# Kernel tuning notes

Measured on AMD Instinct MI355X. Metric: run time of the kernel, lower is better.

The kernel has to match this reference:

```python
import jax, jax.numpy as jnp
import numpy as np

B, T, H, N_HEADS, HEAD_D = 16, 512, 1024, 16, 64
N_SKILLS, N_ITEMS = 50, 1000
VOCAB = 4 + 2 * N_ITEMS  # 2004
LN_EPS = 1e-3            # keras LayerNormalization default
PAD_NEG = -float(2 ** 32)


def position_encoding(length, hidden):
    # official transformer get_position_encoding: [sin | cos], then interleaved
    half = hidden // 2
    pos = jnp.arange(length, dtype=jnp.float32)[:, None]
    log_inc = np.log(1e4) / (half - 1)
    inv_ts = jnp.exp(jnp.arange(half, dtype=jnp.float32) * -log_inc)
    ang = pos * inv_ts[None, :]  # [T, H/2]
    pe = jnp.zeros((length, hidden), dtype=jnp.float32)
    pe = pe.at[:, 0::2].set(jnp.sin(ang))
    pe = pe.at[:, 1::2].set(jnp.cos(ang))
    return pe


def setup_inputs() -> dict:
    key = jax.random.key(0)
    ks = jax.random.split(key, 12)
    rng = np.random.default_rng(0)
    # binary Q-matrix [skills, items]; ensure every item has >=1 skill
    Qb = (rng.random((N_SKILLS, N_ITEMS)) < 0.1).astype(np.float32)
    Qb[rng.integers(0, N_SKILLS, size=N_ITEMS), np.arange(N_ITEMS)] = 1.0
    s = 0.02
    return {
        'prob_x': jax.random.randint(ks[0], (B, T), 4, VOCAB, dtype=jnp.int32),
        'prob_y2': jax.random.randint(ks[1], (B, T), 4, VOCAB, dtype=jnp.int32),
        'emb': jax.random.normal(ks[2], (VOCAB, H), jnp.float32) * s,
        'wq': jax.random.normal(ks[3], (H, N_HEADS, HEAD_D), jnp.float32) * s,
        'wk': jax.random.normal(ks[4], (H, N_HEADS, HEAD_D), jnp.float32) * s,
        'wv': jax.random.normal(ks[5], (H, N_HEADS, HEAD_D), jnp.float32) * s,
        'wo': jax.random.normal(ks[6], (N_HEADS, HEAD_D, H), jnp.float32) * s,
        'ln_gamma': jnp.ones((H,), jnp.float32),
        'ln_beta': jnp.zeros((H,), jnp.float32),
        'w_hid': jax.random.normal(ks[7], (H, 2 * N_SKILLS), jnp.float32) * s,
        'b_hid': jnp.zeros((2 * N_SKILLS,), jnp.float32),
        'w_skill': jax.random.normal(ks[8], (2 * N_SKILLS, N_SKILLS), jnp.float32) * s,
        'b_skill': jnp.zeros((N_SKILLS,), jnp.float32),
        'w_prob': jax.random.normal(ks[9], (N_SKILLS, N_ITEMS), jnp.float32) * s,
        'b_prob': jnp.zeros((N_ITEMS,), jnp.float32),
        'q_matrix': jnp.asarray(Qb),
    }


def reference(prob_x, prob_y2, emb, wq, wk, wv, wo, ln_gamma, ln_beta,
              w_hid, b_hid, w_skill, b_skill, w_prob, b_prob, q_matrix):
    Bq, Tq = prob_x.shape
    pid = (prob_x - 4) // 2        # item ids [B,T]
    next_pid = (prob_y2 - 4) // 2  # [B,T]

    x = emb[prob_x] + position_encoding(Tq, emb.shape[1])  # [B,T,H]

    # QKV projections (DenseEinsum, no bias)
    q = jnp.einsum('bth,hnd->btnd', x, wq) * (HEAD_D ** -0.5)
    k = jnp.einsum('bth,hnd->btnd', x, wk)
    v = jnp.einsum('bth,hnd->btnd', x, wv)

    logits = jnp.einsum('btnd,bfnd->bnft', k, q)  # [B,N,F,T]

    # causal future mask: 0 on/below diag, -inf above (1 - exp(1/tri - 1))
    causal = jnp.where(jnp.tril(jnp.ones((Tq, Tq), bool)), 0.0, -jnp.inf)
    logits = logits + causal[None, None]

    # item-item common-skill mask: -inf where items share no skill, 0 otherwise
    qtq = q_matrix.T @ q_matrix  # [I,I]
    items_items = jnp.where(qtq > 0, 0.0, -jnp.inf)
    sub = items_items[pid[:, 1:, None], pid[:, None, 1:]]  # [B,T-1,T-1]
    csm = jnp.pad(sub, ((0, 0), (1, 0), (1, 0)), constant_values=PAD_NEG)
    logits = logits + csm[:, None]  # broadcast over heads

    weights = jax.nn.softmax(logits, axis=-1)  # [B,N,F,T]
    attn = jnp.einsum('bnft,btnd->bfnd', weights, v)
    attn = jnp.einsum('bfnd,ndh->bfh', attn, wo)

    # add & layer-norm (keras default eps=1e-3)
    y = x + attn
    mu = jnp.mean(y, axis=-1, keepdims=True)
    var = jnp.var(y, axis=-1, keepdims=True)
    y = (y - mu) * jax.lax.rsqrt(var + LN_EPS) * ln_gamma + ln_beta

    h = jax.nn.relu(y @ w_hid + b_hid)
    skills = h @ w_skill + b_skill
    problems = jax.nn.sigmoid(skills @ w_prob + b_prob)  # [B,T,I]
    # einsum('abi,abi->ab', problems, one_hot(next_pid)) == gather
    out = jnp.take_along_axis(problems, next_pid[..., None], axis=-1)[..., 0]
    return out
```

## Files before the change

kernel.cpp:

```cpp
#include <hip/hip_runtime.h>
#include <hip/hip_bf16.h>

#define Bb 16
#define Tt 512
#define Hh 1024
#define NHd 16
#define HD 64
#define BT (Bb*Tt)
#define NSK 50
#define NIT 1000

typedef __attribute__((ext_vector_type(8))) short bf16x8;
typedef __attribute__((ext_vector_type(4))) float f32x4;
typedef unsigned short u16;
typedef unsigned int u32;
typedef unsigned long long u64;

__device__ inline u16 f2bf(float x){
  union { float f; u32 u; } v; v.f = x;
  u32 r = v.u + 0x7fffu + ((v.u >> 16) & 1u);
  return (u16)(r >> 16);
}
__device__ inline float bf2f(u32 u){
  union { u32 uu; float f; } v; v.uu = u << 16; return v.f;
}
__device__ inline u32 pack2bf(float lo, float hi){
  return (u32)f2bf(lo) | ((u32)f2bf(hi) << 16);
}
__device__ inline void gload_lds16(const void* g, void* l){
  __builtin_amdgcn_global_load_lds(
    (const __attribute__((address_space(1))) u32*)g,
    (__attribute__((address_space(3))) u32*)l, 16, 0, 0);
}

__global__ __launch_bounds__(256) void k_wT_all(
    const float* __restrict__ wq, const float* __restrict__ wk,
    const float* __restrict__ wv, const float* __restrict__ wo,
    const float* __restrict__ wh, const float* __restrict__ gamma,
    const float* __restrict__ beta,
    const int* __restrict__ prob_x, const float* __restrict__ qm,
    const float* __restrict__ wp,
    u16* __restrict__ wqkvT, u16* __restrict__ woT, u16* __restrict__ whT,
    float2* __restrict__ uvp, u64* __restrict__ pmask, float* __restrict__ wpt){
  int z = blockIdx.z;
  int tid = threadIdx.x;
  if (z == 5){
    if (blockIdx.y) return;
    int i = blockIdx.x*256 + tid;
    int pid = (prob_x[i] - 4) >> 1;
    u64 m = 0ull;
    #pragma unroll
    for (int s = 0; s < NSK; s++)
      if (qm[s*NIT + pid] != 0.f) m |= (1ull << s);
    pmask[i] = m;
    return;
  }
  if (z == 6){
    int blk = blockIdx.y*32 + blockIdx.x;
    if (blk >= 250) return;
    int p = blk*4 + (tid >> 6), lane = tid & 63;
    if (lane < NSK) wpt[(size_t)p*64 + lane] = wp[(size_t)lane*NIT + p];
    return;
  }
  const float* src; u16* dst; int C = 1024; float scale = 1.f; bool useg = false;
  if      (z == 0){ src = wq; dst = wqkvT;                       scale = 0.125f; }
  else if (z == 1){ src = wk; dst = wqkvT + (size_t)1024*1024; }
  else if (z == 2){ src = wv; dst = wqkvT + (size_t)2*1024*1024; }
  else if (z == 3){ src = wo; dst = woT; }
  else            { src = wh; dst = whT; C = 100; useg = true; if (blockIdx.x >= 4) return; }

  __shared__ float tile[32][33];
  int tx = tid & 31, ty = tid >> 5;
  int c0 = blockIdx.x*32, r0 = blockIdx.y*32;
  #pragma unroll
  for (int i = 0; i < 32; i += 8){
    int r = r0 + ty + i, cc = c0 + tx;
    tile[ty+i][tx] = (cc < C) ? src[(size_t)r*C + cc] : 0.f;
  }
  __syncthreads();
  float gmul = useg ? gamma[r0 + tx] : scale;
  #pragma unroll
  for (int i = 0; i < 32; i += 8){
    int cc = c0 + ty + i, rr = r0 + tx;
    dst[(size_t)cc*1024 + rr] = f2bf(tile[tx][ty+i] * gmul);
  }
  if (useg && tid < 32){
    int j = tid;
    float us = 0.f, vs = 0.f;
    #pragma unroll
    for (int k = 0; k < 32; k++){
      float wv2 = tile[k][j];
      us += gamma[r0 + k] * wv2;
      vs += beta[r0 + k] * wv2;
    }
    uvp[(size_t)blockIdx.y*128 + c0 + j] = make_float2(us, vs);
  }
}

__global__ __launch_bounds__(256) void k_build_x2(
    const int* __restrict__ prob_x, const float* __restrict__ emb,
    u16* __restrict__ xb){
  int bt = blockIdx.x, tid = threadIdx.x;
  int t = bt & (Tt-1);
  int ix = prob_x[bt];
  int h = tid*4;
  float4 e = *(const float4*)(emb + (size_t)ix*Hh + h);
  const float LOG_INC = 0.0180241495f;
  int j0 = h >> 1;
  float a0 = (float)t * __expf(-(float)j0 * LOG_INC);
  float a1 = (float)t * __expf(-(float)(j0+1) * LOG_INC);
  alignas(8) u16 tmp[4] = { f2bf(e.x + __sinf(a0)), f2bf(e.y + __cosf(a0)),
                            f2bf(e.z + __sinf(a1)), f2bf(e.w + __cosf(a1)) };
  *(uint2*)(xb + (size_t)bt*Hh + h) = *(const uint2*)tmp;
}

__global__ __launch_bounds__(256) void k_gemm_qkv(
    const u16* __restrict__ A, const u16* __restrict__ Bt,
    u16* __restrict__ qb, u16* __restrict__ kb, u16* __restrict__ vtb)
{
  __shared__ u16 sA[128*64];
  __shared__ u16 sB[128*64];
  const int tid = threadIdx.x, w = tid >> 6, lane = tid & 63;
  const int c = lane & 15, g = lane >> 4;
  int lin = blockIdx.y*24 + blockIdx.x;
  int id2 = (lin & 7)*192 + (lin >> 3);
  int bx = id2 % 24, by = id2 / 24;
  const int row0 = by*128, col0 = bx*128;
  const int wr = w >> 1, wc = w & 1;
  const int srl = lane >> 3, scb = lane & 7;

  f32x4 acc[4][4];
  #pragma unroll
  for (int mi = 0; mi < 4; mi++)
    #pragma unroll
    for (int ni = 0; ni < 4; ni++) acc[mi][ni] = (f32x4){0.f,0.f,0.f,0.f};

  for (int k0 = 0; k0 < 1024; k0 += 64){
    __syncthreads();
    #pragma unroll
    for (int i = 0; i < 4; i++){
      int arow = 32*w + 8*i + srl;
      int kblk = scb ^ (arow & 7);
      gload_lds16(A  + (size_t)(row0 + arow)*1024 + k0 + kblk*8,
                  (char*)sA + w*4096 + i*1024);
      gload_lds16(Bt + (size_t)(col0 + arow)*1024 + k0 + kblk*8,
                  (char*)sB + w*4096 + i*1024);
    }
    __syncthreads();

    #pragma unroll
    for (int kh = 0; kh < 2; kh++){
      bf16x8 af[4], bf[4];
      #pragma unroll
      for (int mi = 0; mi < 4; mi++){
        int r = 64*wr + 16*mi + c;
        af[mi] = *(const bf16x8*)((char*)sA + r*128 + (((4*kh + g) ^ (r & 7))*16));
      }
      #pragma unroll
      for (int ni = 0; ni < 4; ni++){
        int r = 64*wc + 16*ni + c;
        bf[ni] = *(const bf16x8*)((char*)sB + r*128 + (((4*kh + g) ^ (r & 7))*16));
      }
      #pragma unroll
      for (int mi = 0; mi < 4; mi++)
        #pragma unroll
        for (int ni = 0; ni < 4; ni++)
          acc[mi][ni] = __builtin_amdgcn_mfma_f32_16x16x32_bf16(af[mi], bf[ni], acc[mi][ni], 0, 0, 0);
    }
  }

  int seg = col0 >> 10;
  int colL0 = col0 & 1023;
  if (seg < 2){
    u16* C = seg ? kb : qb;
    #pragma unroll
    for (int mi = 0; mi < 4; mi++){
      int m0 = row0 + 64*wr + 16*mi + 4*g;
      int bb = m0 >> 9, t0 = m0 & (Tt-1);
      #pragma unroll
      for (int ni = 0; ni < 4; ni++){
        int col = colL0 + 64*wc + 16*ni + c;
        int hd_ = col >> 6, d_ = col & 63;
        u16* base = C + (((size_t)bb*NHd + hd_)*Tt + t0)*HD + d_;
        #pragma unroll
        for (int r = 0; r < 4; r++) base[(size_t)r*HD] = f2bf(acc[mi][ni][r]);
      }
    }
  } else {
    #pragma unroll
    for (int mi = 0; mi < 4; mi++){
      int m0 = row0 + 64*wr + 16*mi + 4*g;
      int bb = m0 >> 9, t0 = m0 & (Tt-1);
      #pragma unroll
      for (int ni = 0; ni < 4; ni++){
        int col = colL0 + 64*wc + 16*ni + c;
        int hd_ = col >> 6, d_ = col & 63;
        alignas(8) u16 tmp[4];
        #pragma unroll
        for (int r = 0; r < 4; r++) tmp[r] = f2bf(acc[mi][ni][r]);
        *(uint2*)(vtb + (((size_t)bb*NHd + hd_)*HD + d_)*Tt + t0) = *(const uint2*)tmp;
      }
    }
  }
}

__global__ __launch_bounds__(256) void k_gemm_wo(
    const u16* __restrict__ A, const u16* __restrict__ Bt,
    u16* __restrict__ C, const u16* __restrict__ res, float2* __restrict__ stats)
{
  __shared__ u16 sA[128*64];
  __shared__ u16 sB[128*64];
  const int tid = threadIdx.x, w = tid >> 6, lane = tid & 63;
  const int c = lane & 15, g = lane >> 4;
  int lin = blockIdx.y*8 + blockIdx.x;
  int id2 = (lin & 7)*64 + (lin >> 3);
  int bx = id2 & 7, by = id2 >> 3;
  const int row0 = by*128, col0 = bx*128;
  const int wr = w >> 1, wc = w & 1;
  const int srl = lane >> 3, scb = lane & 7;

  f32x4 acc[4][4];
  #pragma unroll
  for (int mi = 0; mi < 4; mi++)
    #pragma unroll
    for (int ni = 0; ni < 4; ni++) acc[mi][ni] = (f32x4){0.f,0.f,0.f,0.f};

  for (int k0 = 0; k0 < 1024; k0 += 64){
    __syncthreads();
    #pragma unroll
    for (int i = 0; i < 4; i++){
      int arow = 32*w + 8*i + srl;
      int kblk = scb ^ (arow & 7);
      gload_lds16(A  + (size_t)(row0 + arow)*1024 + k0 + kblk*8,
                  (char*)sA + w*4096 + i*1024);
      gload_lds16(Bt + (size_t)(col0 + arow)*1024 + k0 + kblk*8,
                  (char*)sB + w*4096 + i*1024);
    }
    __syncthreads();

    #pragma unroll
    for (int kh = 0; kh < 2; kh++){
      bf16x8 af[4], bf[4];
      #pragma unroll
      for (int mi = 0; mi < 4; mi++){
        int r = 64*wr + 16*mi + c;
        af[mi] = *(const bf16x8*)((char*)sA + r*128 + (((4*kh + g) ^ (r & 7))*16));
      }
      #pragma unroll
      for (int ni = 0; ni < 4; ni++){
        int r = 64*wc + 16*ni + c;
        bf[ni] = *(const bf16x8*)((char*)sB + r*128 + (((4*kh + g) ^ (r & 7))*16));
      }
      #pragma unroll
      for (int mi = 0; mi < 4; mi++)
        #pragma unroll
        for (int ni = 0; ni < 4; ni++)
          acc[mi][ni] = __builtin_amdgcn_mfma_f32_16x16x32_bf16(af[mi], bf[ni], acc[mi][ni], 0, 0, 0);
    }
  }

  __syncthreads();
  float s1[4][4], s2[4][4];
  #pragma unroll
  for (int mi = 0; mi < 4; mi++)
    #pragma unroll
    for (int r = 0; r < 4; r++){ s1[mi][r] = 0.f; s2[mi][r] = 0.f; }

  #pragma unroll
  for (int mi = 0; mi < 4; mi++){
    int m0 = row0 + 64*wr + 16*mi + 4*g;
    #pragma unroll
    for (int ni = 0; ni < 4; ni++){
      int col = col0 + 64*wc + 16*ni + c;
      #pragma unroll
      for (int r = 0; r < 4; r++){
        size_t idx = (size_t)(m0 + r)*Hh + col;
        float yv = acc[mi][ni][r] + bf2f((u32)res[idx]);
        C[idx] = f2bf(yv);
        s1[mi][r] += yv; s2[mi][r] += yv*yv;
      }
    }
  }
  #pragma unroll
  for (int mi = 0; mi < 4; mi++)
    #pragma unroll
    for (int r = 0; r < 4; r++){
      #pragma unroll
      for (int off = 1; off < 16; off <<= 1){
        s1[mi][r] += __shfl_xor(s1[mi][r], off);
        s2[mi][r] += __shfl_xor(s2[mi][r], off);
      }
    }
  float (*sStat)[2][2] = (float(*)[2][2])sA;
  if (c == 0){
    #pragma unroll
    for (int mi = 0; mi < 4; mi++)
      #pragma unroll
      for (int r = 0; r < 4; r++){
        int ml = 64*wr + 16*mi + 4*g + r;
        sStat[ml][wc][0] = s1[mi][r];
        sStat[ml][wc][1] = s2[mi][r];
      }
  }
  __syncthreads();
  if (tid < 128){
    float a = sStat[tid][0][0] + sStat[tid][1][0];
    float b = sStat[tid][0][1] + sStat[tid][1][1];
    stats[(size_t)(row0 + tid)*8 + bx] = make_float2(a, b);
  }
}

__global__ __launch_bounds__(256) void k_gemm_hidden(
    const u16* __restrict__ A, const u16* __restrict__ Bt,
    const float2* __restrict__ stats, const float2* __restrict__ uvp,
    const float* __restrict__ b_hid, u16* __restrict__ C)
{
  __shared__ u16 sA[32*64];
  __shared__ u16 sB[128*64];
  __shared__ float sMu[32][2];
  __shared__ float2 sUV[128];
  const int tid = threadIdx.x, w = tid >> 6, lane = tid & 63;
  const int c = lane & 15, g = lane >> 4;
  const int row0 = blockIdx.x*32;
  const int srl = lane >> 3, scb = lane & 7;

  if (tid < 32){
    float m = 0.f, q = 0.f;
    #pragma unroll
    for (int cb = 0; cb < 8; cb++){
      float2 s = stats[(size_t)(row0 + tid)*8 + cb];
      m += s.x; q += s.y;
    }
    float mu = m * (1.f/Hh);
    float var = q * (1.f/Hh) - mu*mu;
    sMu[tid][0] = mu;
    sMu[tid][1] = rsqrtf(var + 1e-3f);
  }
  if (tid < 128){
    float us = 0.f, vs = 0.f;
    #pragma unroll 8
    for (int cb = 0; cb < 32; cb++){
      float2 p = uvp[(size_t)cb*128 + tid];
      us += p.x; vs += p.y;
    }
    float2 r = make_float2(0.f, 0.f);
    if (tid < 100){ r.x = us; r.y = vs + b_hid[tid]; }
    sUV[tid] = r;
  }

  f32x4 acc[2][2];
  #pragma unroll
  for (int mi = 0; mi < 2; mi++)
    #pragma unroll
    for (int ni = 0; ni < 2; ni++) acc[mi][ni] = (f32x4){0.f,0.f,0.f,0.f};

  for (int k0 = 0; k0 < 1024; k0 += 64){
    __syncthreads();
    {
      int arow = 8*w + srl;
      int kblk = scb ^ (arow & 7);
      gload_lds16(A + (size_t)(row0 + arow)*1024 + k0 + kblk*8,
                  (char*)sA + w*1024);
      #pragma unroll
      for (int i = 0; i < 4; i++){
        int brow = 32*w + 8*i + srl;
        int kb2 = scb ^ (brow & 7);
        gload_lds16(Bt + (size_t)brow*1024 + k0 + kb2*8,
                    (char*)sB + w*4096 + i*1024);
      }
    }
    __syncthreads();

    #pragma unroll
    for (int kh = 0; kh < 2; kh++){
      bf16x8 af[2], bf[2];
      #pragma unroll
      for (int mi = 0; mi < 2; mi++){
        int r = 16*mi + c;
        af[mi] = *(const bf16x8*)((char*)sA + r*128 + (((4*kh + g) ^ (r & 7))*16));
      }
      #pragma unroll
      for (int ni = 0; ni < 2; ni++){
        int r = 32*w + 16*ni + c;
        bf[ni] = *(const bf16x8*)((char*)sB + r*128 + (((4*kh + g) ^ (r & 7))*16));
      }
      #pragma unroll
      for (int mi = 0; mi < 2; mi++)
        #pragma unroll
        for (int ni = 0; ni < 2; ni++)
          acc[mi][ni] = __builtin_amdgcn_mfma_f32_16x16x32_bf16(af[mi], bf[ni], acc[mi][ni], 0, 0, 0);
    }
  }

  #pragma unroll
  for (int mi = 0; mi < 2; mi++){
    #pragma unroll
    for (int ni = 0; ni < 2; ni++){
      int col = 32*w + 16*ni + c;
      float2 uvv = sUV[col];
      #pragma unroll
      for (int r = 0; r < 4; r++){
        int ml = 16*mi + 4*g + r;
        float mu = sMu[ml][0], inv = sMu[ml][1];
        float h = fmaxf(inv*(acc[mi][ni][r] - mu*uvv.x) + uvv.y, 0.f);
        C[(size_t)(row0 + ml)*128 + col] = f2bf(h);
      }
    }
  }
}

__global__ __launch_bounds__(256, 3) void k_flash(
    const u16* __restrict__ qb, const u16* __restrict__ kb,
    const u16* __restrict__ vtb, const u64* __restrict__ pmask,
    u16* __restrict__ o)
{
  __shared__ u16 sK[2][64*64];
  __shared__ u16 sV[2][64*64];
  __shared__ u16 sP[4][32*64];

  const int tid = threadIdx.x;
  const int w = tid >> 6, lane = tid & 63;
  const int c = lane & 15, g = lane >> 4;
  const int bn = blockIdx.x;
  const int Fblk = 3 - blockIdx.y;
  const int b = bn >> 4, n = bn & 15;
  const int f0w = Fblk*128 + w*32;

  bf16x8 qf[2][2];
  #pragma unroll
  for (int fb = 0; fb < 2; fb++){
    const u16* qrow = qb + ((size_t)bn*Tt + f0w + 16*fb + c)*HD + 8*g;
    qf[fb][0] = *(const bf16x8*)(qrow);
    qf[fb][1] = *(const bf16x8*)(qrow + 32);
  }

  const u64* pmb = pmask + b*Tt;
  int frow[2]; u64 mf[2];
  #pragma unroll
  for (int fb = 0; fb < 2; fb++){ frow[fb] = f0w + 16*fb + c; mf[fb] = pmb[frow[fb]]; }

  f32x4 O[2][4];
  #pragma unroll
  for (int fb = 0; fb < 2; fb++)
    #pragma unroll
    for (int dt = 0; dt < 4; dt++) O[fb][dt] = (f32x4){0.f,0.f,0.f,0.f};
  float m_run[2] = {-1e30f, -1e30f};
  float l_run[2] = {0.f, 0.f};

  const char* kbase = (const char*)(kb + (size_t)bn*Tt*HD);
  const char* vbase = (const char*)(vtb + (size_t)bn*HD*Tt);
  char* sPw = (char*)(sP[w]);

  const int srow0 = 16*w + (lane >> 3);
  const int scb = lane & 7;

  #define STAGE(buf, T0)                                                          \
    {                                                                             \
      _Pragma("unroll")                                                           \
      for (int i = 0; i < 2; i++){                                                \
        int row = srow0 + 8*i;                                                    \
        int cb = scb ^ (row & 7);                                                 \
        gload_lds16(kbase + (size_t)((T0) + row)*128 + cb*16,                     \
                    (char*)sK[buf] + w*2048 + i*1024);                            \
        gload_lds16(vbase + (size_t)row*1024 + (T0)*2 + cb*16,                    \
                    (char*)sV[buf] + w*2048 + i*1024);                            \
      }                                                                           \
    }

  const int nT = 2*Fblk + 2;
  STAGE(0, 0)
  __syncthreads();
  int cur = 0;

  for (int it = 0; it < nT; ++it){
    const int t0 = it * 64;
    if (it + 1 < nT) STAGE(cur^1, (it+1)*64)

    if (t0 <= f0w + 31){
      const char* sKc = (const char*)sK[cur];
      const char* sVc = (const char*)sV[cur];

      f32x4 S[2][4];
      __builtin_amdgcn_s_setprio(1);
      #pragma unroll
      for (int ts = 0; ts < 4; ts++){
        int tl = ts*16 + c;
        const char* kr = sKc + tl*128;
        int sw = (tl & 7) << 4;
        bf16x8 kf0 = *(const bf16x8*)(kr + ((g*16) ^ sw));
        bf16x8 kf1 = *(const bf16x8*)(kr + ((64 + g*16) ^ sw));
        #pragma unroll
        for (int fb = 0; fb < 2; fb++){
          f32x4 a = (f32x4){0.f,0.f,0.f,0.f};
          a = __builtin_amdgcn_mfma_f32_16x16x32_bf16(kf0, qf[fb][0], a, 0, 0, 0);
          a = __builtin_amdgcn_mfma_f32_16x16x32_bf16(kf1, qf[fb][1], a, 0, 0, 0);
          S[fb][ts] = a;
        }
      }
      __builtin_amdgcn_s_setprio(0);

      u64 pmt[4][4];
      #pragma unroll
      for (int ts = 0; ts < 4; ts++){
        const u64* pp = pmb + t0 + 16*ts + 4*g;
        pmt[ts][0] = pp[0]; pmt[ts][1] = pp[1];
        pmt[ts][2] = pp[2]; pmt[ts][3] = pp[3];
      }

      #pragma unroll
      for (int fb = 0; fb < 2; fb++){
        int f = frow[fb];
        u64 mfr = mf[fb];
        #pragma unroll
        for (int ts = 0; ts < 4; ts++){
          #pragma unroll
          for (int r = 0; r < 4; r++){
            int t = t0 + 16*ts + 4*g + r;
            bool ok = (f == 0) ? (t == 0)
                     : (t > 0 && t <= f && ((pmt[ts][r] & mfr) != 0ull));
            if (!ok) S[fb][ts][r] = -1e30f;
          }
        }
        float mx = -1e30f;
        #pragma unroll
        for (int ts = 0; ts < 4; ts++)
          #pragma unroll
          for (int r = 0; r < 4; r++) mx = fmaxf(mx, S[fb][ts][r]);
        mx = fmaxf(mx, __shfl_xor(mx, 16));
        mx = fmaxf(mx, __shfl_xor(mx, 32));
        float mnew = fmaxf(m_run[fb], mx);
        float al = __expf(m_run[fb] - mnew);
        m_run[fb] = mnew;
        l_run[fb] *= al;
        #pragma unroll
        for (int dt = 0; dt < 4; dt++) O[fb][dt] *= al;

        int prow = 16*fb + c;
        int swz = (prow & 7) << 4;
        float lsum = 0.f;
        #pragma unroll
        for (int ts = 0; ts < 4; ts++){
          float p0 = __expf(S[fb][ts][0] - mnew);
          float p1 = __expf(S[fb][ts][1] - mnew);
          float p2 = __expf(S[fb][ts][2] - mnew);
          float p3 = __expf(S[fb][ts][3] - mnew);
          lsum += (p0 + p1) + (p2 + p3);
          uint2 dw = { pack2bf(p0, p1), pack2bf(p2, p3) };
          *(uint2*)(sPw + prow*128 + ((32*ts + 8*g) ^ swz)) = dw;
        }
        l_run[fb] += lsum;
      }

      bf16x8 pa[2][2];
      #pragma unroll
      for (int fb = 0; fb < 2; fb++){
        int prow = 16*fb + c;
        int swz = (prow & 7) << 4;
        const char* pr = sPw + prow*128;
        pa[fb][0] = *(const bf16x8*)(pr + ((16*g) ^ swz));
        pa[fb][1] = *(const bf16x8*)(pr + ((64 + 16*g) ^ swz));
      }
      __builtin_amdgcn_s_setprio(1);
      #pragma unroll
      for (int dt = 0; dt < 4; dt++){
        int vl = dt*16 + c;
        const char* vr = sVc + vl*128;
        int swv = (vl & 7) << 4;
        bf16x8 vf0 = *(const bf16x8*)(vr + ((g*16) ^ swv));
        bf16x8 vf1 = *(const bf16x8*)(vr + ((64 + g*16) ^ swv));
        #pragma unroll
        for (int fb = 0; fb < 2; fb++){
          O[fb][dt] = __builtin_amdgcn_mfma_f32_16x16x32_bf16(vf0, pa[fb][0], O[fb][dt], 0, 0, 0);
          O[fb][dt] = __builtin_amdgcn_mfma_f32_16x16x32_bf16(vf1, pa[fb][1], O[fb][dt], 0, 0, 0);
        }
      }
      __builtin_amdgcn_s_setprio(0);
    }

    __syncthreads();
    cur ^= 1;
  }
  #undef STAGE

  #pragma unroll
  for (int fb = 0; fb < 2; fb++){
    float l = l_run[fb];
    l += __shfl_xor(l, 16);
    l += __shfl_xor(l, 32);
    float inv = 1.f / l;
    u16* ob = o + ((size_t)(b*Tt + frow[fb]))*Hh + n*HD;
    #pragma unroll
    for (int dt = 0; dt < 4; dt++){
      alignas(8) u16 tmp[4];
      #pragma unroll
      for (int r = 0; r < 4; r++) tmp[r] = f2bf(O[fb][dt][r] * inv);
      *(uint2*)(ob + dt*16 + 4*g) = *(const uint2*)tmp;
    }
  }
}

__global__ __launch_bounds__(256) void k_tail(
    const u16* __restrict__ hidden, const int* __restrict__ prob_y2,
    const float* __restrict__ w_skill, const float* __restrict__ b_skill,
    const float* __restrict__ wpt, const float* __restrict__ b_prob,
    float* __restrict__ out)
{
  __shared__ float shid[4][104];
  int w = threadIdx.x >> 6, lane = threadIdx.x & 63;
  int row = blockIdx.x*4 + w;
  if (lane < 50){
    u32 hp = *(const u32*)(hidden + (size_t)row*128 + 2*lane);
    shid[w][2*lane]   = bf2f(hp & 0xffffu);
    shid[w][2*lane+1] = bf2f(hp >> 16);
  }
  __syncthreads();
  float s = 0.f;
  if (lane < 50){
    s = b_skill[lane];
    #pragma unroll 4
    for (int i = 0; i < 100; i++) s += shid[w][i] * w_skill[i*NSK + lane];
  }
  int np = (prob_y2[row] - 4) >> 1;
  float z = (lane < 50) ? s * wpt[(size_t)np*64 + lane] : 0.f;
  #pragma unroll
  for (int off = 1; off < 64; off <<= 1) z += __shfl_xor(z, off);
  if (lane == 0) out[row] = 1.f/(1.f + expf(-(z + b_prob[np])));
}

extern "C" void kernel_launch(void* const* d_in, const int* in_sizes, int n_in,
                              void* d_out, int out_size, void* d_ws, size_t ws_size,
                              hipStream_t stream)
{
  const int*   prob_x   = (const int*)d_in[0];
  const int*   prob_y2  = (const int*)d_in[1];
  const float* emb      = (const float*)d_in[2];
  const float* wq       = (const float*)d_in[3];
  const float* wk       = (const float*)d_in[4];
  const float* wv       = (const float*)d_in[5];
  const float* wo       = (const float*)d_in[6];
  const float* ln_g     = (const float*)d_in[7];
  const float* ln_b     = (const float*)d_in[8];
  const float* w_hid    = (const float*)d_in[9];
  const float* b_hid    = (const float*)d_in[10];
  const float* w_skill  = (const float*)d_in[11];
  const float* b_skill  = (const float*)d_in[12];
  const float* w_prob   = (const float*)d_in[13];
  const float* b_prob   = (const float*)d_in[14];
  const float* q_matrix = (const float*)d_in[15];
  float* out = (float*)d_out;

  char* ws = (char*)d_ws;
  const size_t M16 = (size_t)BT*Hh*2;
  u16*   xb     = (u16*)(ws);
  u16*   qb     = (u16*)(ws + M16);
  u16*   kb     = (u16*)(ws + 2*M16);
  u16*   vtb    = (u16*)(ws + 3*M16);
  u16*   att    = (u16*)(ws + 4*M16);
  u16*   y      = qb;
  u16*   hidden = kb;
  char*  aux    = ws + 5*M16;
  u16*   wqkvT  = (u16*)(aux);
  u16*   woT    = wqkvT + (size_t)3*1024*1024;
  u16*   whT    = woT + (size_t)1024*1024;
  float* wpt    = (float*)(whT + (size_t)128*1024);
  u64*   pmask  = (u64*)(wpt + (size_t)NIT*64);
  float2* stats = (float2*)((char*)pmask + (size_t)BT*8);
  float2* uvp   = (float2*)((char*)stats + (size_t)BT*8*sizeof(float2));

  k_wT_all<<<dim3(32,32,7), 256, 0, stream>>>(wq, wk, wv, wo, w_hid, ln_g, ln_b,
                                              prob_x, q_matrix, w_prob,
                                              wqkvT, woT, whT, uvp, pmask, wpt);
  k_build_x2<<<BT, 256, 0, stream>>>(prob_x, emb, xb);

  k_gemm_qkv<<<dim3(24,64), 256, 0, stream>>>(xb, wqkvT, qb, kb, vtb);

  k_flash<<<dim3(Bb*NHd, 4), 256, 0, stream>>>(qb, kb, vtb, pmask, att);

  k_gemm_wo<<<dim3(8,64), 256, 0, stream>>>(att, woT, y, xb, stats);

  k_gemm_hidden<<<256, 256, 0, stream>>>(y, whT, stats, uvp, b_hid, hidden);

  k_tail<<<BT/4, 256, 0, stream>>>(hidden, prob_y2, w_skill, b_skill, wpt, b_prob, out);
}
```

Baseline: 180.7 us.

## Rewrite QKV GEMM with 256x256 tiles, 8 waves, double-buffered LDS pipeline

```diff
diff --git a/kernel.cpp b/kernel.cpp
--- a/kernel.cpp
+++ b/kernel.cpp
@@ -114,72 +114,139 @@
   *(uint2*)(xb + (size_t)bt*Hh + h) = *(const uint2*)tmp;
 }
 
-__global__ __launch_bounds__(256) void k_gemm_qkv(
+#define MFMA_(d, va, vb) d = __builtin_amdgcn_mfma_f32_16x16x32_bf16(va, vb, d, 0, 0, 0)
+
+__global__ __launch_bounds__(512, 2) void k_gemm_qkv8(
     const u16* __restrict__ A, const u16* __restrict__ Bt,
     u16* __restrict__ qb, u16* __restrict__ kb, u16* __restrict__ vtb)
 {
-  __shared__ u16 sA[128*64];
-  __shared__ u16 sB[128*64];
+  extern __shared__ char lds[];
   const int tid = threadIdx.x, w = tid >> 6, lane = tid & 63;
   const int c = lane & 15, g = lane >> 4;
-  int lin = blockIdx.y*24 + blockIdx.x;
-  int id2 = (lin & 7)*192 + (lin >> 3);
-  int bx = id2 % 24, by = id2 / 24;
-  const int row0 = by*128, col0 = bx*128;
-  const int wr = w >> 1, wc = w & 1;
+  const int wm = w >> 2, wn = w & 3;
   const int srl = lane >> 3, scb = lane & 7;
 
-  f32x4 acc[4][4];
-  #pragma unroll
-  for (int mi = 0; mi < 4; mi++)
+  int lin = blockIdx.x;
+  int swz = (lin & 7)*48 + (lin >> 3);
+  int bx = swz % 12, by = swz / 12;
+  const int row0 = by*256, col0 = bx*256;
+
+  f32x4 acc[8][4];
+  #pragma unroll
+  for (int mi = 0; mi < 8; mi++)
     #pragma unroll
     for (int ni = 0; ni < 4; ni++) acc[mi][ni] = (f32x4){0.f,0.f,0.f,0.f};
 
-  for (int k0 = 0; k0 < 1024; k0 += 64){
-    __syncthreads();
-    #pragma unroll
-    for (int i = 0; i < 4; i++){
-      int arow = 32*w + 8*i + srl;
-      int kblk = scb ^ (arow & 7);
-      gload_lds16(A  + (size_t)(row0 + arow)*1024 + k0 + kblk*8,
-                  (char*)sA + w*4096 + i*1024);
-      gload_lds16(Bt + (size_t)(col0 + arow)*1024 + k0 + kblk*8,
-                  (char*)sB + w*4096 + i*1024);
-    }
-    __syncthreads();
-
-    #pragma unroll
-    for (int kh = 0; kh < 2; kh++){
-      bf16x8 af[4], bf[4];
-      #pragma unroll
-      for (int mi = 0; mi < 4; mi++){
-        int r = 64*wr + 16*mi + c;
-        af[mi] = *(const bf16x8*)((char*)sA + r*128 + (((4*kh + g) ^ (r & 7))*16));
-      }
-      #pragma unroll
-      for (int ni = 0; ni < 4; ni++){
-        int r = 64*wc + 16*ni + c;
-        bf[ni] = *(const bf16x8*)((char*)sB + r*128 + (((4*kh + g) ^ (r & 7))*16));
-      }
-      #pragma unroll
-      for (int mi = 0; mi < 4; mi++)
-        #pragma unroll
-        for (int ni = 0; ni < 4; ni++)
-          acc[mi][ni] = __builtin_amdgcn_mfma_f32_16x16x32_bf16(af[mi], bf[ni], acc[mi][ni], 0, 0, 0);
-    }
-  }
+  #define STAGEH(buf, mat, h, k0)                                               \
+    do {                                                                        \
+      const u16* _s = (mat) ? Bt : A;                                           \
+      int _b0 = (mat) ? col0 : row0;                                            \
+      char* _d = lds + (buf)*65536 + (mat)*32768 + (h)*16384 + w*2048;          \
+      int _kb = scb ^ srl;                                                      \
+      gload_lds16(_s + (size_t)(_b0 + (h)*128 + w*16 + srl)*1024 + (k0) + _kb*8,\
+                  _d);                                                          \
+      gload_lds16(_s + (size_t)(_b0 + (h)*128 + w*16 + 8 + srl)*1024 + (k0) + _kb*8,\
+                  _d + 1024);                                                   \
+    } while (0)
+
+  #define AFRAG(buf, mi, kh)                                                    \
+    (*(const bf16x8*)(lds + (buf)*65536 + (128*wm + 16*(mi) + c)*128 +          \
+                      ((((kh)*4 + g) ^ (c & 7))*16)))
+  #define BFRAG(buf, ni, kh)                                                    \
+    (*(const bf16x8*)(lds + (buf)*65536 + 32768 + (64*wn + 16*(ni) + c)*128 +   \
+                      ((((kh)*4 + g) ^ (c & 7))*16)))
+
+  STAGEH(0, 0, 0, 0); STAGEH(0, 0, 1, 0);
+  STAGEH(0, 1, 0, 0); STAGEH(0, 1, 1, 0);
+
+  bf16x8 af[4], bfr[4];
+
+  for (int kt = 0; kt < 16; ++kt){
+    const int buf = kt & 1, nbuf = buf ^ 1;
+    const int k0n = (kt + 1)*64;
+    const bool pf = (kt < 15);
+
+    if (pf){
+      STAGEH(nbuf, 0, 0, k0n);
+      asm volatile("s_waitcnt vmcnt(2)" ::: "memory");
+    } else {
+      asm volatile("s_waitcnt vmcnt(0)" ::: "memory");
+    }
+    __builtin_amdgcn_sched_barrier(0);
+    __builtin_amdgcn_s_barrier();
+    #pragma unroll
+    for (int mi = 0; mi < 4; mi++) af[mi] = AFRAG(buf, mi, 0);
+    #pragma unroll
+    for (int ni = 0; ni < 4; ni++) bfr[ni] = BFRAG(buf, ni, 0);
+    asm volatile("s_waitcnt lgkmcnt(0)" ::: "memory");
+    __builtin_amdgcn_sched_barrier(0);
+    __builtin_amdgcn_s_setprio(1);
+    #pragma unroll
+    for (int mi = 0; mi < 4; mi++)
+      #pragma unroll
+      for (int ni = 0; ni < 4; ni++) MFMA_(acc[mi][ni], af[mi], bfr[ni]);
+    __builtin_amdgcn_s_setprio(0);
+    __builtin_amdgcn_s_barrier();
+
+    #pragma unroll
+    for (int mi = 0; mi < 4; mi++) af[mi] = AFRAG(buf, 4 + mi, 0);
+    if (pf) STAGEH(nbuf, 0, 1, k0n);
+    __builtin_amdgcn_s_barrier();
+    asm volatile("s_waitcnt lgkmcnt(0)" ::: "memory");
+    __builtin_amdgcn_sched_barrier(0);
+    __builtin_amdgcn_s_setprio(1);
+    #pragma unroll
+    for (int mi = 0; mi < 4; mi++)
+      #pragma unroll
+      for (int ni = 0; ni < 4; ni++) MFMA_(acc[4 + mi][ni], af[mi], bfr[ni]);
+    __builtin_amdgcn_s_setprio(0);
+    __builtin_amdgcn_s_barrier();
+
+    #pragma unroll
+    for (int mi = 0; mi < 4; mi++) af[mi] = AFRAG(buf, mi, 1);
+    #pragma unroll
+    for (int ni = 0; ni < 4; ni++) bfr[ni] = BFRAG(buf, ni, 1);
+    if (pf) STAGEH(nbuf, 1, 0, k0n);
+    __builtin_amdgcn_s_barrier();
+    asm volatile("s_waitcnt lgkmcnt(0)" ::: "memory");
+    __builtin_amdgcn_sched_barrier(0);
+    __builtin_amdgcn_s_setprio(1);
+    #pragma unroll
+    for (int mi = 0; mi < 4; mi++)
+      #pragma unroll
+      for (int ni = 0; ni < 4; ni++) MFMA_(acc[mi][ni], af[mi], bfr[ni]);
+    __builtin_amdgcn_s_setprio(0);
+    __builtin_amdgcn_s_barrier();
+
+    #pragma unroll
+    for (int mi = 0; mi < 4; mi++) af[mi] = AFRAG(buf, 4 + mi, 1);
+    if (pf) STAGEH(nbuf, 1, 1, k0n);
+    __builtin_amdgcn_s_barrier();
+    asm volatile("s_waitcnt lgkmcnt(0)" ::: "memory");
+    __builtin_amdgcn_sched_barrier(0);
+    __builtin_amdgcn_s_setprio(1);
+    #pragma unroll
+    for (int mi = 0; mi < 4; mi++)
+      #pragma unroll
+      for (int ni = 0; ni < 4; ni++) MFMA_(acc[4 + mi][ni], af[mi], bfr[ni]);
+    __builtin_amdgcn_s_setprio(0);
+    __builtin_amdgcn_s_barrier();
+  }
+  #undef STAGEH
+  #undef AFRAG
+  #undef BFRAG
 
   int seg = col0 >> 10;
   int colL0 = col0 & 1023;
   if (seg < 2){
     u16* C = seg ? kb : qb;
     #pragma unroll
-    for (int mi = 0; mi < 4; mi++){
-      int m0 = row0 + 64*wr + 16*mi + 4*g;
+    for (int mi = 0; mi < 8; mi++){
+      int m0 = row0 + 128*wm + 16*mi + 4*g;
       int bb = m0 >> 9, t0 = m0 & (Tt-1);
       #pragma unroll
       for (int ni = 0; ni < 4; ni++){
-        int col = colL0 + 64*wc + 16*ni + c;
+        int col = colL0 + 64*wn + 16*ni + c;
         int hd_ = col >> 6, d_ = col & 63;
         u16* base = C + (((size_t)bb*NHd + hd_)*Tt + t0)*HD + d_;
         #pragma unroll
@@ -188,12 +255,12 @@
     }
   } else {
     #pragma unroll
-    for (int mi = 0; mi < 4; mi++){
-      int m0 = row0 + 64*wr + 16*mi + 4*g;
+    for (int mi = 0; mi < 8; mi++){
+      int m0 = row0 + 128*wm + 16*mi + 4*g;
       int bb = m0 >> 9, t0 = m0 & (Tt-1);
       #pragma unroll
       for (int ni = 0; ni < 4; ni++){
-        int col = colL0 + 64*wc + 16*ni + c;
+        int col = colL0 + 64*wn + 16*ni + c;
         int hd_ = col >> 6, d_ = col & 63;
         alignas(8) u16 tmp[4];
         #pragma unroll
@@ -672,7 +739,7 @@
                                               wqkvT, woT, whT, uvp, pmask, wpt);
   k_build_x2<<<BT, 256, 0, stream>>>(prob_x, emb, xb);
 
-  k_gemm_qkv<<<dim3(24,64), 256, 0, stream>>>(xb, wqkvT, qb, kb, vtb);
+  k_gemm_qkv8<<<384, 512, 131072, stream>>>(xb, wqkvT, qb, kb, vtb);
 
   k_flash<<<dim3(Bb*NHd, 4), 256, 0, stream>>>(qb, kb, vtb, pmask, att);
 
```

After: 175.5 us. 1.03x faster.

## Use triple-buffered 128x256 GEMM core with 512 threads for QKV and Wo

Applied to the files above, without the earlier changes.

```diff
diff --git a/kernel.cpp b/kernel.cpp
--- a/kernel.cpp
+++ b/kernel.cpp
@@ -114,72 +114,108 @@
   *(uint2*)(xb + (size_t)bt*Hh + h) = *(const uint2*)tmp;
 }
 
-__global__ __launch_bounds__(256) void k_gemm_qkv(
+#define MFMA_(d, va, vb) d = __builtin_amdgcn_mfma_f32_16x16x32_bf16(va, vb, d, 0, 0, 0)
+
+__device__ __forceinline__ void gemm128x256_core(
+    const u16* __restrict__ A, const u16* __restrict__ Bt,
+    int row0, int col0, char* lds, f32x4 (&acc)[4][4])
+{
+  const int tid = threadIdx.x, w = tid >> 6, lane = tid & 63;
+  const int c = lane & 15, g = lane >> 4;
+  const int wm = w >> 2, wn = w & 3;
+  const int srl = lane >> 3, scb = lane & 7;
+  const int kbsw = scb ^ srl;
+
+  #define STAGE6(buf, k0)                                                        \
+    do {                                                                         \
+      char* _da = lds + (buf)*49152 + w*2048;                                    \
+      char* _db = lds + (buf)*49152 + 16384 + w*4096;                            \
+      _Pragma("unroll")                                                          \
+      for (int i = 0; i < 2; i++)                                                \
+        gload_lds16(A + (size_t)(row0 + 16*w + 8*i + srl)*1024 + (k0) + kbsw*8,  \
+                    _da + i*1024);                                               \
+      _Pragma("unroll")                                                          \
+      for (int i = 0; i < 4; i++)                                                \
+        gload_lds16(Bt + (size_t)(col0 + 32*w + 8*i + srl)*1024 + (k0) + kbsw*8, \
+                    _db + i*1024);                                               \
+    } while (0)
+
+  STAGE6(0, 0);
+  STAGE6(1, 64);
+  asm volatile("s_waitcnt vmcnt(6)" ::: "memory");
+  __builtin_amdgcn_sched_barrier(0);
+  __builtin_amdgcn_s_barrier();
+
+  #pragma unroll
+  for (int kt = 0; kt < 16; ++kt){
+    const int buf = kt % 3;
+    if (kt + 2 < 16) STAGE6((kt + 2) % 3, (kt + 2)*64);
+
+    #pragma unroll
+    for (int kh = 0; kh < 2; kh++){
+      bf16x8 af[4], bf[4];
+      #pragma unroll
+      for (int mi = 0; mi < 4; mi++){
+        int r = 64*wm + 16*mi + c;
+        af[mi] = *(const bf16x8*)(lds + buf*49152 + r*128 + (((kh*4 + g) ^ (c & 7))*16));
+      }
+      #pragma unroll
+      for (int ni = 0; ni < 4; ni++){
+        int r = 64*wn + 16*ni + c;
+        bf[ni] = *(const bf16x8*)(lds + buf*49152 + 16384 + r*128 + (((kh*4 + g) ^ (c & 7))*16));
+      }
+      asm volatile("s_waitcnt lgkmcnt(0)" ::: "memory");
+      __builtin_amdgcn_sched_barrier(0);
+      __builtin_amdgcn_s_setprio(1);
+      #pragma unroll
+      for (int mi = 0; mi < 4; mi++)
+        #pragma unroll
+        for (int ni = 0; ni < 4; ni++) MFMA_(acc[mi][ni], af[mi], bf[ni]);
+      __builtin_amdgcn_s_setprio(0);
+    }
+
+    if (kt < 15){
+      if (kt < 14) asm volatile("s_waitcnt vmcnt(6)" ::: "memory");
+      else         asm volatile("s_waitcnt vmcnt(0)" ::: "memory");
+      __builtin_amdgcn_sched_barrier(0);
+      __builtin_amdgcn_s_barrier();
+    }
+  }
+  #undef STAGE6
+}
+
+__global__ __launch_bounds__(512) void k_gemm_qkv3(
     const u16* __restrict__ A, const u16* __restrict__ Bt,
     u16* __restrict__ qb, u16* __restrict__ kb, u16* __restrict__ vtb)
 {
-  __shared__ u16 sA[128*64];
-  __shared__ u16 sB[128*64];
+  extern __shared__ char lds[];
+  int lin = blockIdx.x;
+  int swz = (lin & 7)*96 + (lin >> 3);
+  int bx = swz % 12, by = swz / 12;
+  const int row0 = by*128, col0 = bx*256;
+
+  f32x4 acc[4][4];
+  #pragma unroll
+  for (int mi = 0; mi < 4; mi++)
+    #pragma unroll
+    for (int ni = 0; ni < 4; ni++) acc[mi][ni] = (f32x4){0.f,0.f,0.f,0.f};
+
+  gemm128x256_core(A, Bt, row0, col0, lds, acc);
+
   const int tid = threadIdx.x, w = tid >> 6, lane = tid & 63;
   const int c = lane & 15, g = lane >> 4;
-  int lin = blockIdx.y*24 + blockIdx.x;
-  int id2 = (lin & 7)*192 + (lin >> 3);
-  int bx = id2 % 24, by = id2 / 24;
-  const int row0 = by*128, col0 = bx*128;
-  const int wr = w >> 1, wc = w & 1;
-  const int srl = lane >> 3, scb = lane & 7;
-
-  f32x4 acc[4][4];
-  #pragma unroll
-  for (int mi = 0; mi < 4; mi++)
-    #pragma unroll
-    for (int ni = 0; ni < 4; ni++) acc[mi][ni] = (f32x4){0.f,0.f,0.f,0.f};
-
-  for (int k0 = 0; k0 < 1024; k0 += 64){
-    __syncthreads();
-    #pragma unroll
-    for (int i = 0; i < 4; i++){
-      int arow = 32*w + 8*i + srl;
-      int kblk = scb ^ (arow & 7);
-      gload_lds16(A  + (size_t)(row0 + arow)*1024 + k0 + kblk*8,
-                  (char*)sA + w*4096 + i*1024);
-      gload_lds16(Bt + (size_t)(col0 + arow)*1024 + k0 + kblk*8,
-                  (char*)sB + w*4096 + i*1024);
-    }
-    __syncthreads();
-
-    #pragma unroll
-    for (int kh = 0; kh < 2; kh++){
-      bf16x8 af[4], bf[4];
-      #pragma unroll
-      for (int mi = 0; mi < 4; mi++){
-        int r = 64*wr + 16*mi + c;
-        af[mi] = *(const bf16x8*)((char*)sA + r*128 + (((4*kh + g) ^ (r & 7))*16));
-      }
-      #pragma unroll
-      for (int ni = 0; ni < 4; ni++){
-        int r = 64*wc + 16*ni + c;
-        bf[ni] = *(const bf16x8*)((char*)sB + r*128 + (((4*kh + g) ^ (r & 7))*16));
-      }
-      #pragma unroll
-      for (int mi = 0; mi < 4; mi++)
-        #pragma unroll
-        for (int ni = 0; ni < 4; ni++)
-          acc[mi][ni] = __builtin_amdgcn_mfma_f32_16x16x32_bf16(af[mi], bf[ni], acc[mi][ni], 0, 0, 0);
-    }
-  }
-
+  const int wm = w >> 2, wn = w & 3;
   int seg = col0 >> 10;
   int colL0 = col0 & 1023;
   if (seg < 2){
     u16* C = seg ? kb : qb;
     #pragma unroll
     for (int mi = 0; mi < 4; mi++){
-      int m0 = row0 + 64*wr + 16*mi + 4*g;
+      int m0 = row0 + 64*wm + 16*mi + 4*g;
       int bb = m0 >> 9, t0 = m0 & (Tt-1);
       #pragma unroll
       for (int ni = 0; ni < 4; ni++){
-        int col = colL0 + 64*wc + 16*ni + c;
+        int col = colL0 + 64*wn + 16*ni + c;
         int hd_ = col >> 6, d_ = col & 63;
         u16* base = C + (((size_t)bb*NHd + hd_)*Tt + t0)*HD + d_;
         #pragma unroll
@@ -189,11 +225,11 @@
   } else {
     #pragma unroll
     for (int mi = 0; mi < 4; mi++){
-      int m0 = row0 + 64*wr + 16*mi + 4*g;
+      int m0 = row0 + 64*wm + 16*mi + 4*g;
       int bb = m0 >> 9, t0 = m0 & (Tt-1);
       #pragma unroll
       for (int ni = 0; ni < 4; ni++){
-        int col = colL0 + 64*wc + 16*ni + c;
+        int col = colL0 + 64*wn + 16*ni + c;
         int hd_ = col >> 6, d_ = col & 63;
         alignas(8) u16 tmp[4];
         #pragma unroll
@@ -204,74 +240,40 @@
   }
 }
 
-__global__ __launch_bounds__(256) void k_gemm_wo(
+__global__ __launch_bounds__(512) void k_gemm_wo3(
     const u16* __restrict__ A, const u16* __restrict__ Bt,
     u16* __restrict__ C, const u16* __restrict__ res, float2* __restrict__ stats)
 {
-  __shared__ u16 sA[128*64];
-  __shared__ u16 sB[128*64];
+  extern __shared__ char lds[];
+  int lin = blockIdx.x;
+  int swz = (lin & 7)*32 + (lin >> 3);
+  int bx = swz & 3, by = swz >> 2;
+  const int row0 = by*128, col0 = bx*256;
+
+  f32x4 acc[4][4];
+  #pragma unroll
+  for (int mi = 0; mi < 4; mi++)
+    #pragma unroll
+    for (int ni = 0; ni < 4; ni++) acc[mi][ni] = (f32x4){0.f,0.f,0.f,0.f};
+
+  gemm128x256_core(A, Bt, row0, col0, lds, acc);
+
   const int tid = threadIdx.x, w = tid >> 6, lane = tid & 63;
   const int c = lane & 15, g = lane >> 4;
-  int lin = blockIdx.y*8 + blockIdx.x;
-  int id2 = (lin & 7)*64 + (lin >> 3);
-  int bx = id2 & 7, by = id2 >> 3;
-  const int row0 = by*128, col0 = bx*128;
-  const int wr = w >> 1, wc = w & 1;
-  const int srl = lane >> 3, scb = lane & 7;
-
-  f32x4 acc[4][4];
+  const int wm = w >> 2, wn = w & 3;
+
+  float s1[4][4], s2[4][4];
   #pragma unroll
   for (int mi = 0; mi < 4; mi++)
     #pragma unroll
-    for (int ni = 0; ni < 4; ni++) acc[mi][ni] = (f32x4){0.f,0.f,0.f,0.f};
-
-  for (int k0 = 0; k0 < 1024; k0 += 64){
-    __syncthreads();
-    #pragma unroll
-    for (int i = 0; i < 4; i++){
-      int arow = 32*w + 8*i + srl;
-      int kblk = scb ^ (arow & 7);
-      gload_lds16(A  + (size_t)(row0 + arow)*1024 + k0 + kblk*8,
-                  (char*)sA + w*4096 + i*1024);
-      gload_lds16(Bt + (size_t)(col0 + arow)*1024 + k0 + kblk*8,
-                  (char*)sB + w*4096 + i*1024);
-    }
-    __syncthreads();
-
-    #pragma unroll
-    for (int kh = 0; kh < 2; kh++){
-      bf16x8 af[4], bf[4];
-      #pragma unroll
-      for (int mi = 0; mi < 4; mi++){
-        int r = 64*wr + 16*mi + c;
-        af[mi] = *(const bf16x8*)((char*)sA + r*128 + (((4*kh + g) ^ (r & 7))*16));
-      }
-      #pragma unroll
-      for (int ni = 0; ni < 4; ni++){
-        int r = 64*wc + 16*ni + c;
-        bf[ni] = *(const bf16x8*)((char*)sB + r*128 + (((4*kh + g) ^ (r & 7))*16));
-      }
-      #pragma unroll
-      for (int mi = 0; mi < 4; mi++)
-        #pragma unroll
-        for (int ni = 0; ni < 4; ni++)
-          acc[mi][ni] = __builtin_amdgcn_mfma_f32_16x16x32_bf16(af[mi], bf[ni], acc[mi][ni], 0, 0, 0);
-    }
-  }
-
-  __syncthreads();
-  float s1[4][4], s2[4][4];
-  #pragma unroll
-  for (int mi = 0; mi < 4; mi++)
-    #pragma unroll
     for (int r = 0; r < 4; r++){ s1[mi][r] = 0.f; s2[mi][r] = 0.f; }
 
   #pragma unroll
   for (int mi = 0; mi < 4; mi++){
-    int m0 = row0 + 64*wr + 16*mi + 4*g;
+    int m0 = row0 + 64*wm + 16*mi + 4*g;
     #pragma unroll
     for (int ni = 0; ni < 4; ni++){
-      int col = col0 + 64*wc + 16*ni + c;
+      int col = col0 + 64*wn + 16*ni + c;
       #pragma unroll
       for (int r = 0; r < 4; r++){
         size_t idx = (size_t)(m0 + r)*Hh + col;
@@ -291,22 +293,23 @@
         s2[mi][r] += __shfl_xor(s2[mi][r], off);
       }
     }
-  float (*sStat)[2][2] = (float(*)[2][2])sA;
+  __syncthreads();
+  float (*sStat)[4][2] = (float(*)[4][2])lds;
   if (c == 0){
     #pragma unroll
     for (int mi = 0; mi < 4; mi++)
       #pragma unroll
       for (int r = 0; r < 4; r++){
-        int ml = 64*wr + 16*mi + 4*g + r;
-        sStat[ml][wc][0] = s1[mi][r];
-        sStat[ml][wc][1] = s2[mi][r];
+        int ml = 64*wm + 16*mi + 4*g + r;
+        sStat[ml][wn][0] = s1[mi][r];
+        sStat[ml][wn][1] = s2[mi][r];
       }
   }
   __syncthreads();
   if (tid < 128){
-    float a = sStat[tid][0][0] + sStat[tid][1][0];
-    float b = sStat[tid][0][1] + sStat[tid][1][1];
-    stats[(size_t)(row0 + tid)*8 + bx] = make_float2(a, b);
+    float a = sStat[tid][0][0] + sStat[tid][1][0] + sStat[tid][2][0] + sStat[tid][3][0];
+    float b = sStat[tid][0][1] + sStat[tid][1][1] + sStat[tid][2][1] + sStat[tid][3][1];
+    stats[(size_t)(row0 + tid)*4 + bx] = make_float2(a, b);
   }
 }
 
@@ -327,8 +330,8 @@
   if (tid < 32){
     float m = 0.f, q = 0.f;
     #pragma unroll
-    for (int cb = 0; cb < 8; cb++){
-      float2 s = stats[(size_t)(row0 + tid)*8 + cb];
+    for (int cb = 0; cb < 4; cb++){
+      float2 s = stats[(size_t)(row0 + tid)*4 + cb];
       m += s.x; q += s.y;
     }
     float mu = m * (1.f/Hh);
@@ -672,11 +675,11 @@
                                               wqkvT, woT, whT, uvp, pmask, wpt);
   k_build_x2<<<BT, 256, 0, stream>>>(prob_x, emb, xb);
 
-  k_gemm_qkv<<<dim3(24,64), 256, 0, stream>>>(xb, wqkvT, qb, kb, vtb);
+  k_gemm_qkv3<<<768, 512, 147456, stream>>>(xb, wqkvT, qb, kb, vtb);
 
   k_flash<<<dim3(Bb*NHd, 4), 256, 0, stream>>>(qb, kb, vtb, pmask, att);
 
-  k_gemm_wo<<<dim3(8,64), 256, 0, stream>>>(att, woT, y, xb, stats);
+  k_gemm_wo3<<<256, 512, 147456, stream>>>(att, woT, y, xb, stats);
 
   k_gemm_hidden<<<256, 256, 0, stream>>>(y, whT, stats, uvp, b_hid, hidden);
 
```

After: 173.9 us. 3.8% less time.
